# Kernel optimization log

Measured on AMD Instinct MI355X. Metric: run time of the kernel, lower is better.

## Reference

```python
import jax, jax.numpy as jnp
import numpy as np


def _he_scale(k, shape, fan_in):
    return jax.random.normal(k, shape, dtype=jnp.float32) * np.sqrt(2.0 / fan_in).astype(np.float32)


def setup_inputs() -> dict:
    key = jax.random.key(0)
    kx, kt, kp, kg, kf = jax.random.split(key, 5)
    B, H, W, C, D = 4, 64, 64, 256, 128
    x = jax.random.normal(kx, (B, H, W, C), dtype=jnp.float32)
    Wt = _he_scale(kt, (C, D), C)
    Wp = _he_scale(kp, (C, D), C)
    Wg = _he_scale(kg, (C, D), C)
    Wf = _he_scale(kf, (D, C), D)
    return {"x": x, "Wt": Wt, "Wp": Wp, "Wg": Wg, "Wf": Wf}


def _maxpool1d(z, pool_size=2, stride=1):
    # Keras MaxPool1D, padding='valid': output length = (N - pool_size)//stride + 1
    return jax.lax.reduce_window(
        z, -jnp.inf, jax.lax.max,
        window_dimensions=(1, pool_size, 1),
        window_strides=(1, stride, 1),
        padding='VALID')


def reference(x, Wt, Wp, Wg, Wf):
    B, H, W, C = x.shape
    D = Wt.shape[1]
    N = H * W
    # 1x1 conv projections == per-position matmuls
    theta = jnp.einsum('bhwc,cd->bhwd', x, Wt).reshape(B, N, D)   # [B,N,D]
    phi = jnp.einsum('bhwc,cd->bhwd', x, Wp).reshape(B, N, D)     # [B,N,D]
    g = jnp.einsum('bhwc,cd->bhwd', x, Wg).reshape(B, N, D)       # [B,N,D]
    # embedded mode: subsample phi and g (pool_size=2, strides=1) -> M = N-1
    phi = _maxpool1d(phi)                                          # [B,M,D]
    g = _maxpool1d(g)                                              # [B,M,D]
    # f = theta @ phi^T, softmax over keys (no scaling in embedded mode)
    f = jax.nn.softmax(jnp.einsum('bnd,bmd->bnm', theta, phi), axis=-1)  # [B,N,M]
    y = jnp.einsum('bnm,bmd->bnd', f, g).reshape(B, H, W, D)       # [B,H,W,D]
    # final 1x1 conv back to C channels + residual
    z = x + jnp.einsum('bhwd,dc->bhwc', y, Wf)
    return z
```

## Files before the change

### kernel.cpp

```cpp
#include <hip/hip_runtime.h>

#define B_  4
#define N_  4096
#define C_  256
#define D_  128
#define M_  4095
#define BN_ (B_ * N_)
#define KSPLIT 4
#define KEYS_PER_SPLIT (N_ / KSPLIT)
#define KTILES (KEYS_PER_SPLIT / 64)

typedef _Float16 half_t;
typedef __attribute__((ext_vector_type(8))) _Float16 half8;
typedef __attribute__((ext_vector_type(4))) _Float16 half4;
typedef __attribute__((ext_vector_type(4))) float f32x4;

#define MFMA16x16x32(A, B, C) __builtin_amdgcn_mfma_f32_16x16x32_f16(A, B, C, 0, 0, 0)
#define LOG2E 1.44269504088896f

__global__ __launch_bounds__(256) void prep_kernel(
    const float* __restrict__ Wt, const float* __restrict__ Wp,
    const float* __restrict__ Wg, const float* __restrict__ Wf,
    half_t* __restrict__ WT_hi, half_t* __restrict__ WT_lo,
    half_t* __restrict__ WfT)
{
    const int idx = blockIdx.x * 256 + threadIdx.x;
    const int wsel = blockIdx.y;
    if (wsel < 3) {
        const float* __restrict__ W = (wsel == 0) ? Wt : (wsel == 1) ? Wp : Wg;
        const int d = idx >> 8, c = idx & 255;
        const float v = W[(size_t)c * D_ + d];
        const half_t h = (half_t)v;
        WT_hi[(size_t)wsel * 32768 + idx] = h;
        WT_lo[(size_t)wsel * 32768 + idx] = (half_t)(v - (float)h);
    } else {
        const int c = idx >> 7, d = idx & 127;
        WfT[idx] = (half_t)Wf[(size_t)d * C_ + c];
    }
}

__global__ __launch_bounds__(256) void proj_kernel(
    const float* __restrict__ x, const half_t* __restrict__ WT_hi,
    const half_t* __restrict__ WT_lo, half_t* __restrict__ theta,
    half_t* __restrict__ pphi, half_t* __restrict__ pgT)
{
    const int tid = threadIdx.x;
    const int lane = tid & 63;
    const int w = tid >> 6;
    const int lm = lane & 15;
    const int lq = lane >> 4;
    const int r0 = blockIdx.x * 128;
    const int which = blockIdx.y;
    const half_t* __restrict__ Wh_g = WT_hi + (size_t)which * 32768;
    const half_t* __restrict__ Wl_g = WT_lo + (size_t)which * 32768;

    __shared__ __align__(16) unsigned char lds_raw[40960];
    half_t (*Xh)[40]  = (half_t (*)[40])(lds_raw);
    half_t (*Xl)[40]  = (half_t (*)[40])(lds_raw + 10240);
    half_t (*Whl)[40] = (half_t (*)[40])(lds_raw + 20480);
    half_t (*Wll)[40] = (half_t (*)[40])(lds_raw + 30720);

    f32x4 acc[2][8];
#pragma unroll
    for (int rb = 0; rb < 2; ++rb)
#pragma unroll
        for (int nb = 0; nb < 8; ++nb)
#pragma unroll
            for (int r = 0; r < 4; ++r) acc[rb][nb][r] = 0.f;

    const int sr = tid >> 1;
    const int cL = (tid & 1) * 16;

    for (int kc = 0; kc < 8; ++kc) {
        __syncthreads();
        {
            const float* xs = x + (size_t)(r0 + sr) * C_ + kc * 32 + cL;
            float vv[16];
            float4 v0 = *(const float4*)&xs[0], v1 = *(const float4*)&xs[4];
            float4 v2 = *(const float4*)&xs[8], v3 = *(const float4*)&xs[12];
            vv[0]=v0.x; vv[1]=v0.y; vv[2]=v0.z; vv[3]=v0.w;
            vv[4]=v1.x; vv[5]=v1.y; vv[6]=v1.z; vv[7]=v1.w;
            vv[8]=v2.x; vv[9]=v2.y; vv[10]=v2.z; vv[11]=v2.w;
            vv[12]=v3.x; vv[13]=v3.y; vv[14]=v3.z; vv[15]=v3.w;
            half8 hi[2], lo[2];
#pragma unroll
            for (int j = 0; j < 16; ++j) {
                half_t h = (half_t)vv[j];
                hi[j >> 3][j & 7] = h;
                lo[j >> 3][j & 7] = (half_t)(vv[j] - (float)h);
            }
            *(half8*)&Xh[sr][cL] = hi[0]; *(half8*)&Xh[sr][cL + 8] = hi[1];
            *(half8*)&Xl[sr][cL] = lo[0]; *(half8*)&Xl[sr][cL + 8] = lo[1];
            const half_t* wh = Wh_g + (size_t)sr * 256 + kc * 32 + cL;
            const half_t* wl = Wl_g + (size_t)sr * 256 + kc * 32 + cL;
            *(half8*)&Whl[sr][cL] = *(const half8*)&wh[0];
            *(half8*)&Whl[sr][cL + 8] = *(const half8*)&wh[8];
            *(half8*)&Wll[sr][cL] = *(const half8*)&wl[0];
            *(half8*)&Wll[sr][cL + 8] = *(const half8*)&wl[8];
        }
        __syncthreads();

        half8 ah[2], al[2];
#pragma unroll
        for (int rb = 0; rb < 2; ++rb) {
            ah[rb] = *(const half8*)&Xh[w * 32 + rb * 16 + lm][lq * 8];
            al[rb] = *(const half8*)&Xl[w * 32 + rb * 16 + lm][lq * 8];
        }
#pragma unroll
        for (int nb = 0; nb < 8; ++nb) {
            half8 bh = *(const half8*)&Whl[nb * 16 + lm][lq * 8];
            half8 bl = *(const half8*)&Wll[nb * 16 + lm][lq * 8];
#pragma unroll
            for (int rb = 0; rb < 2; ++rb) {
                acc[rb][nb] = MFMA16x16x32(ah[rb], bh, acc[rb][nb]);
                acc[rb][nb] = MFMA16x16x32(al[rb], bh, acc[rb][nb]);
                acc[rb][nb] = MFMA16x16x32(ah[rb], bl, acc[rb][nb]);
            }
        }
    }

    if (which == 0) {
#pragma unroll
        for (int rb = 0; rb < 2; ++rb)
#pragma unroll
            for (int nb = 0; nb < 8; ++nb)
#pragma unroll
                for (int r = 0; r < 4; ++r)
                    theta[(size_t)(r0 + w * 32 + rb * 16 + lq * 4 + r) * D_ +
                          nb * 16 + lm] = (half_t)(acc[rb][nb][r] * LOG2E);
        return;
    }

    __syncthreads();
    half_t (*LsT)[136] = (half_t (*)[136])(lds_raw);
#pragma unroll
    for (int rb = 0; rb < 2; ++rb)
#pragma unroll
        for (int nb = 0; nb < 8; ++nb) {
            const int d = nb * 16 + lm;
            const int m = w * 32 + rb * 16 + lq * 4;
            half4 pk;
#pragma unroll
            for (int r = 0; r < 4; ++r) pk[r] = (half_t)acc[rb][nb][r];
            *(half4*)&LsT[d][m] = pk;
        }
    if (tid < 128) {
        int rh = r0 + 128;
        if ((rh & (N_ - 1)) == 0) rh = r0 + 127;
        const float* xr = x + (size_t)rh * C_;
        const half_t* wh = Wh_g + (size_t)tid * 256;
        const half_t* wl = Wl_g + (size_t)tid * 256;
        float s = 0.f;
#pragma unroll
        for (int c8 = 0; c8 < 32; ++c8) {
            half8 h = *(const half8*)&wh[c8 * 8];
            half8 l = *(const half8*)&wl[c8 * 8];
            float4 xa = *(const float4*)&xr[c8 * 8];
            float4 xb = *(const float4*)&xr[c8 * 8 + 4];
            s += xa.x * ((float)h[0] + (float)l[0]) + xa.y * ((float)h[1] + (float)l[1])
               + xa.z * ((float)h[2] + (float)l[2]) + xa.w * ((float)h[3] + (float)l[3])
               + xb.x * ((float)h[4] + (float)l[4]) + xb.y * ((float)h[5] + (float)l[5])
               + xb.z * ((float)h[6] + (float)l[6]) + xb.w * ((float)h[7] + (float)l[7]);
        }
        LsT[tid][128] = (half_t)s;
    }
    __syncthreads();

    if (which == 1) {
        const int m = tid >> 1, dh = (tid & 1) * 64;
        half8 o[8];
#pragma unroll
        for (int j = 0; j < 64; ++j) {
            float v0 = (float)LsT[dh + j][m];
            float v1 = (float)LsT[dh + j][m + 1];
            o[j >> 3][j & 7] = (half_t)fmaxf(v0, v1);
        }
        half8* dst = (half8*)&pphi[(size_t)(r0 + m) * D_ + dh];
#pragma unroll
        for (int j = 0; j < 8; ++j) dst[j] = o[j];
    } else {
        const int d = tid >> 1, mh = (tid & 1) * 64;
        const int b = r0 / N_, m0 = r0 & (N_ - 1);
        half8 in[8];
#pragma unroll
        for (int j = 0; j < 8; ++j) in[j] = *(const half8*)&LsT[d][mh + j * 8];
        const half_t ext = LsT[d][mh + 64];
        half8 o[8];
#pragma unroll
        for (int j = 0; j < 64; ++j) {
            float v0 = (float)in[j >> 3][j & 7];
            float v1 = (j == 63) ? (float)ext : (float)in[(j + 1) >> 3][(j + 1) & 7];
            o[j >> 3][j & 7] = (half_t)fmaxf(v0, v1);
        }
        half8* dst = (half8*)&pgT[((size_t)b * D_ + d) * N_ + m0 + mh];
#pragma unroll
        for (int j = 0; j < 8; ++j) dst[j] = o[j];
    }
}

__global__ __launch_bounds__(256, 2) void attn_kernel(
    const half_t* __restrict__ theta, const half_t* __restrict__ pphi,
    const half_t* __restrict__ pgT, half_t* __restrict__ ypart,
    float* __restrict__ mstat, float* __restrict__ lstat)
{
    const int tid = threadIdx.x;
    const int lane = tid & 63;
    const int w = tid >> 6;
    const int lm = lane & 15;
    const int lq = lane >> 4;
    const int qt = blockIdx.x, ksb = blockIdx.y, b = blockIdx.z;
    const int q0 = qt * 128;

    __shared__ half_t Ks[64][136];
    __shared__ half_t Gts[128][72];
    __shared__ half_t Ps[128][72];

    half8 qh[2][4];
#pragma unroll
    for (int nb = 0; nb < 2; ++nb) {
        const half_t* tr_ = theta + ((size_t)b * N_ + q0 + w * 32 + nb * 16 + lm) * D_;
#pragma unroll
        for (int k4 = 0; k4 < 4; ++k4)
            qh[nb][k4] = *(const half8*)(tr_ + k4 * 32 + lq * 8);
    }

    float m_i[2] = {-1e30f, -1e30f};
    float l_i[2] = {0.f, 0.f};
    f32x4 yacc[2][8];
#pragma unroll
    for (int mb = 0; mb < 2; ++mb)
#pragma unroll
        for (int dn = 0; dn < 8; ++dn)
#pragma unroll
            for (int r = 0; r < 4; ++r) yacc[mb][dn][r] = 0.f;

    for (int kt = 0; kt < KTILES; ++kt) {
        const int k0 = ksb * KEYS_PER_SPLIT + kt * 64;
        __syncthreads();
        {
            const int key = tid >> 2, ch = (tid & 3);
            const float4* src = (const float4*)(pphi +
                ((size_t)b * N_ + k0 + key) * D_ + ch * 32);
            float4 a0 = src[0], a1 = src[1], a2 = src[2], a3 = src[3];
            float4* dst = (float4*)&Ks[key][ch * 32];
            dst[0] = a0; dst[1] = a1; dst[2] = a2; dst[3] = a3;
            const int d = tid >> 1, kh = (tid & 1);
            const float4* gs = (const float4*)(pgT +
                ((size_t)b * D_ + d) * N_ + k0 + kh * 32);
            float4 g0 = gs[0], g1 = gs[1], g2 = gs[2], g3 = gs[3];
            float4* gd = (float4*)&Gts[d][kh * 32];
            gd[0] = g0; gd[1] = g1; gd[2] = g2; gd[3] = g3;
        }
        __syncthreads();

        f32x4 sc[4][2];
#pragma unroll
        for (int kb = 0; kb < 4; ++kb)
#pragma unroll
            for (int nb = 0; nb < 2; ++nb)
#pragma unroll
                for (int r = 0; r < 4; ++r) sc[kb][nb][r] = 0.f;
#pragma unroll
        for (int kb = 0; kb < 4; ++kb) {
#pragma unroll
            for (int k4 = 0; k4 < 4; ++k4) {
                half8 kf = *(const half8*)&Ks[kb * 16 + lm][k4 * 32 + lq * 8];
#pragma unroll
                for (int nb = 0; nb < 2; ++nb)
                    sc[kb][nb] = MFMA16x16x32(kf, qh[nb][k4], sc[kb][nb]);
            }
        }
        if (k0 + 64 > M_) {
#pragma unroll
            for (int kb = 0; kb < 4; ++kb)
#pragma unroll
                for (int r = 0; r < 4; ++r)
                    if (k0 + kb * 16 + lq * 4 + r >= M_) {
                        sc[kb][0][r] = -1e30f; sc[kb][1][r] = -1e30f;
                    }
        }
        float alpha[2];
#pragma unroll
        for (int nb = 0; nb < 2; ++nb) {
            float mt = -1e30f;
#pragma unroll
            for (int kb = 0; kb < 4; ++kb)
#pragma unroll
                for (int r = 0; r < 4; ++r) mt = fmaxf(mt, sc[kb][nb][r]);
            mt = fmaxf(mt, __shfl_xor(mt, 16, 64));
            mt = fmaxf(mt, __shfl_xor(mt, 32, 64));
            const float mnew = fmaxf(m_i[nb], mt);
            alpha[nb] = exp2f(m_i[nb] - mnew);
            m_i[nb] = mnew;
            float rs = 0.f;
#pragma unroll
            for (int kb = 0; kb < 4; ++kb)
#pragma unroll
                for (int r = 0; r < 4; ++r) {
                    float p = exp2f(sc[kb][nb][r] - mnew);
                    sc[kb][nb][r] = p;
                    rs += p;
                }
            rs += __shfl_xor(rs, 16, 64);
            rs += __shfl_xor(rs, 32, 64);
            l_i[nb] = l_i[nb] * alpha[nb] + rs;
#pragma unroll
            for (int kb = 0; kb < 4; ++kb) {
                half4 pk;
#pragma unroll
                for (int r = 0; r < 4; ++r) pk[r] = (half_t)sc[kb][nb][r];
                *(half4*)&Ps[w * 32 + nb * 16 + lm][kb * 16 + lq * 4] = pk;
            }
        }
        float alpha_t[2][4];
#pragma unroll
        for (int mb = 0; mb < 2; ++mb)
#pragma unroll
            for (int r = 0; r < 4; ++r)
                alpha_t[mb][r] = __shfl(alpha[mb], lq * 4 + r, 16);
#pragma unroll
        for (int mb = 0; mb < 2; ++mb)
#pragma unroll
            for (int dn = 0; dn < 8; ++dn)
#pragma unroll
                for (int r = 0; r < 4; ++r) yacc[mb][dn][r] *= alpha_t[mb][r];
        half8 pf[2][2];
#pragma unroll
        for (int mb = 0; mb < 2; ++mb)
#pragma unroll
            for (int k2 = 0; k2 < 2; ++k2)
                pf[mb][k2] = *(const half8*)&Ps[w * 32 + mb * 16 + lm][k2 * 32 + lq * 8];
#pragma unroll
        for (int dn = 0; dn < 8; ++dn) {
#pragma unroll
            for (int k2 = 0; k2 < 2; ++k2) {
                half8 gf = *(const half8*)&Gts[dn * 16 + lm][k2 * 32 + lq * 8];
                yacc[0][dn] = MFMA16x16x32(pf[0][k2], gf, yacc[0][dn]);
                yacc[1][dn] = MFMA16x16x32(pf[1][k2], gf, yacc[1][dn]);
            }
        }
    }

    half_t* yp = ypart + ((size_t)ksb * BN_ + (size_t)b * N_) * D_;
#pragma unroll
    for (int mb = 0; mb < 2; ++mb)
#pragma unroll
        for (int dn = 0; dn < 8; ++dn)
#pragma unroll
            for (int r = 0; r < 4; ++r)
                yp[(size_t)(q0 + w * 32 + mb * 16 + lq * 4 + r) * D_ + dn * 16 + lm] =
                    (half_t)yacc[mb][dn][r];
    if (lq == 0) {
#pragma unroll
        for (int nb = 0; nb < 2; ++nb) {
            const int row = q0 + w * 32 + nb * 16 + lm;
            mstat[(size_t)ksb * BN_ + (size_t)b * N_ + row] = m_i[nb];
            lstat[(size_t)ksb * BN_ + (size_t)b * N_ + row] = l_i[nb];
        }
    }
}

__global__ __launch_bounds__(256) void final_kernel(
    const half_t* __restrict__ ypart, const float* __restrict__ mstat,
    const float* __restrict__ lstat, const float* __restrict__ x,
    const half_t* __restrict__ WfT, float* __restrict__ out)
{
    const int tid = threadIdx.x;
    const int lane = tid & 63;
    const int w = tid >> 6;
    const int lm = lane & 15;
    const int lq = lane >> 4;
    const int r0 = blockIdx.x * 128;
    const int c0 = blockIdx.y * 128;

    __shared__ half_t Ys[128][72];
    __shared__ half_t Wfs[128][72];
    __shared__ float scl[4][128];

    if (tid < 128) {
        const int row = r0 + tid;
        float mv[4], lv[4], wv[4];
        float Mx = -1e30f;
#pragma unroll
        for (int s = 0; s < 4; ++s) {
            mv[s] = mstat[(size_t)s * BN_ + row];
            lv[s] = lstat[(size_t)s * BN_ + row];
            Mx = fmaxf(Mx, mv[s]);
        }
        float lsum = 0.f;
#pragma unroll
        for (int s = 0; s < 4; ++s) { wv[s] = exp2f(mv[s] - Mx); lsum += wv[s] * lv[s]; }
        const float inv = 1.f / lsum;
#pragma unroll
        for (int s = 0; s < 4; ++s) scl[s][tid] = wv[s] * inv;
    }
    __syncthreads();

    f32x4 acc[2][8];
#pragma unroll
    for (int rb = 0; rb < 2; ++rb)
#pragma unroll
        for (int nb = 0; nb < 8; ++nb)
#pragma unroll
            for (int r = 0; r < 4; ++r) acc[rb][nb][r] = 0.f;

    const int sr = tid >> 1;
    const int dd = (tid & 1) * 32;

    for (int kc = 0; kc < 2; ++kc) {
        {
            const float s0 = scl[0][sr], s1 = scl[1][sr],
                        s2 = scl[2][sr], s3 = scl[3][sr];
            const size_t yb = (size_t)(r0 + sr) * D_ + kc * 64 + dd;
            half8 o[4];
#pragma unroll
            for (int q = 0; q < 4; ++q) {
                half8 y0 = *(const half8*)&ypart[0 * (size_t)BN_ * D_ + yb + q * 8];
                half8 y1 = *(const half8*)&ypart[1 * (size_t)BN_ * D_ + yb + q * 8];
                half8 y2 = *(const half8*)&ypart[2 * (size_t)BN_ * D_ + yb + q * 8];
                half8 y3 = *(const half8*)&ypart[3 * (size_t)BN_ * D_ + yb + q * 8];
#pragma unroll
                for (int j = 0; j < 8; ++j)
                    o[q][j] = (half_t)(s0 * (float)y0[j] + s1 * (float)y1[j] +
                                       s2 * (float)y2[j] + s3 * (float)y3[j]);
            }
#pragma unroll
            for (int q = 0; q < 4; ++q) *(half8*)&Ys[sr][dd + q * 8] = o[q];
            const half_t* wf = WfT + (size_t)(c0 + sr) * D_ + kc * 64 + dd;
#pragma unroll
            for (int q = 0; q < 4; ++q)
                *(half8*)&Wfs[sr][dd + q * 8] = *(const half8*)&wf[q * 8];
        }
        __syncthreads();

        half8 af[2][2];
#pragma unroll
        for (int rb = 0; rb < 2; ++rb)
#pragma unroll
            for (int k2 = 0; k2 < 2; ++k2)
                af[rb][k2] = *(const half8*)&Ys[w * 32 + rb * 16 + lm][k2 * 32 + lq * 8];
#pragma unroll
        for (int nb = 0; nb < 8; ++nb) {
#pragma unroll
            for (int k2 = 0; k2 < 2; ++k2) {
                half8 bf = *(const half8*)&Wfs[nb * 16 + lm][k2 * 32 + lq * 8];
                acc[0][nb] = MFMA16x16x32(af[0][k2], bf, acc[0][nb]);
                acc[1][nb] = MFMA16x16x32(af[1][k2], bf, acc[1][nb]);
            }
        }
        __syncthreads();
    }
#pragma unroll
    for (int rb = 0; rb < 2; ++rb)
#pragma unroll
        for (int nb = 0; nb < 8; ++nb)
#pragma unroll
            for (int r = 0; r < 4; ++r) {
                const int row = r0 + w * 32 + rb * 16 + lq * 4 + r;
                const int col = c0 + nb * 16 + lm;
                out[(size_t)row * C_ + col] =
                    acc[rb][nb][r] + x[(size_t)row * C_ + col];
            }
}

extern "C" void kernel_launch(void* const* d_in, const int* in_sizes, int n_in,
                              void* d_out, int out_size, void* d_ws, size_t ws_size,
                              hipStream_t stream)
{
    const float* x  = (const float*)d_in[0];
    const float* Wt = (const float*)d_in[1];
    const float* Wp = (const float*)d_in[2];
    const float* Wg = (const float*)d_in[3];
    const float* Wf = (const float*)d_in[4];
    float* out = (float*)d_out;

    const size_t SEG = (size_t)BN_ * D_;
    float* ws     = (float*)d_ws;
    half_t* theta = (half_t*)ws;
    half_t* pphi  = (half_t*)(ws + SEG / 2);
    half_t* pgT   = (half_t*)(ws + SEG);
    half_t* ypart = (half_t*)(ws + SEG + SEG / 2);
    float* mstat  = ws + 3 * SEG + SEG / 2;
    float* lstat  = mstat + (size_t)KSPLIT * BN_;
    half_t* WT_hi = (half_t*)(lstat + (size_t)KSPLIT * BN_);
    half_t* WT_lo = WT_hi + 3 * 32768;
    half_t* WfT   = WT_lo + 3 * 32768;

    prep_kernel<<<dim3(128, 4), 256, 0, stream>>>(Wt, Wp, Wg, Wf, WT_hi, WT_lo, WfT);
    proj_kernel<<<dim3(BN_ / 128, 3), 256, 0, stream>>>(x, WT_hi, WT_lo,
                                                        theta, pphi, pgT);
    attn_kernel<<<dim3(N_ / 128, KSPLIT, B_), 256, 0, stream>>>(
        theta, pphi, pgT, ypart, mstat, lstat);
    final_kernel<<<dim3(BN_ / 128, 2), 256, 0, stream>>>(
        ypart, mstat, lstat, x, WfT, out);
}
```

Before: 187.7 us.

## Split attention keys six ways with uneven ranges and raise occupancy

Attention now splits the key range into six chunks instead of four. Chunk boundaries are computed from tile indices, so splits can be uneven (10 or 11 tiles each), which puts more blocks on the GPU. Launch bounds are raised to three blocks per SM, and the per-tile cross-lane row-sum reduction is deferred to a single reduction at the end. The combine kernel is generalized to KSPLIT partials, and the workspace layout grows to hold six partial outputs. The cost is more ypart memory traffic in the final kernel and possible register pressure at the higher occupancy target.

```diff
diff --git a/kernel.cpp b/kernel.cpp
--- a/kernel.cpp
+++ b/kernel.cpp
@@ -6,9 +6,7 @@
 #define D_  128
 #define M_  4095
 #define BN_ (B_ * N_)
-#define KSPLIT 4
-#define KEYS_PER_SPLIT (N_ / KSPLIT)
-#define KTILES (KEYS_PER_SPLIT / 64)
+#define KSPLIT 6
 
 typedef _Float16 half_t;
 typedef __attribute__((ext_vector_type(8))) _Float16 half8;
@@ -198,7 +196,7 @@
     }
 }
 
-__global__ __launch_bounds__(256, 2) void attn_kernel(
+__global__ __launch_bounds__(256, 3) void attn_kernel(
     const half_t* __restrict__ theta, const half_t* __restrict__ pphi,
     const half_t* __restrict__ pgT, half_t* __restrict__ ypart,
     float* __restrict__ mstat, float* __restrict__ lstat)
@@ -210,6 +208,8 @@
     const int lq = lane >> 4;
     const int qt = blockIdx.x, ksb = blockIdx.y, b = blockIdx.z;
     const int q0 = qt * 128;
+    const int kt0 = (64 * ksb) / KSPLIT;
+    const int kt1 = (64 * (ksb + 1)) / KSPLIT;
 
     __shared__ half_t Ks[64][136];
     __shared__ half_t Gts[128][72];
@@ -234,8 +234,8 @@
 #pragma unroll
             for (int r = 0; r < 4; ++r) yacc[mb][dn][r] = 0.f;
 
-    for (int kt = 0; kt < KTILES; ++kt) {
-        const int k0 = ksb * KEYS_PER_SPLIT + kt * 64;
+    for (int kt = kt0; kt < kt1; ++kt) {
+        const int k0 = kt * 64;
         __syncthreads();
         {
             const int key = tid >> 2, ch = (tid & 3);
@@ -301,8 +301,6 @@
                     sc[kb][nb][r] = p;
                     rs += p;
                 }
-            rs += __shfl_xor(rs, 16, 64);
-            rs += __shfl_xor(rs, 32, 64);
             l_i[nb] = l_i[nb] * alpha[nb] + rs;
 #pragma unroll
             for (int kb = 0; kb < 4; ++kb) {
@@ -341,6 +339,11 @@
         }
     }
 
+#pragma unroll
+    for (int nb = 0; nb < 2; ++nb) {
+        l_i[nb] += __shfl_xor(l_i[nb], 16, 64);
+        l_i[nb] += __shfl_xor(l_i[nb], 32, 64);
+    }
     half_t* yp = ypart + ((size_t)ksb * BN_ + (size_t)b * N_) * D_;
 #pragma unroll
     for (int mb = 0; mb < 2; ++mb)
@@ -375,24 +378,24 @@
 
     __shared__ half_t Ys[128][72];
     __shared__ half_t Wfs[128][72];
-    __shared__ float scl[4][128];
+    __shared__ float scl[KSPLIT][128];
 
     if (tid < 128) {
         const int row = r0 + tid;
-        float mv[4], lv[4], wv[4];
+        float mv[KSPLIT], lv[KSPLIT], wv[KSPLIT];
         float Mx = -1e30f;
 #pragma unroll
-        for (int s = 0; s < 4; ++s) {
+        for (int s = 0; s < KSPLIT; ++s) {
             mv[s] = mstat[(size_t)s * BN_ + row];
             lv[s] = lstat[(size_t)s * BN_ + row];
             Mx = fmaxf(Mx, mv[s]);
         }
         float lsum = 0.f;
 #pragma unroll
-        for (int s = 0; s < 4; ++s) { wv[s] = exp2f(mv[s] - Mx); lsum += wv[s] * lv[s]; }
+        for (int s = 0; s < KSPLIT; ++s) { wv[s] = exp2f(mv[s] - Mx); lsum += wv[s] * lv[s]; }
         const float inv = 1.f / lsum;
 #pragma unroll
-        for (int s = 0; s < 4; ++s) scl[s][tid] = wv[s] * inv;
+        for (int s = 0; s < KSPLIT; ++s) scl[s][tid] = wv[s] * inv;
     }
     __syncthreads();
 
@@ -409,20 +412,24 @@
 
     for (int kc = 0; kc < 2; ++kc) {
         {
-            const float s0 = scl[0][sr], s1 = scl[1][sr],
-                        s2 = scl[2][sr], s3 = scl[3][sr];
+            float ss[KSPLIT];
+#pragma unroll
+            for (int s = 0; s < KSPLIT; ++s) ss[s] = scl[s][sr];
             const size_t yb = (size_t)(r0 + sr) * D_ + kc * 64 + dd;
             half8 o[4];
 #pragma unroll
             for (int q = 0; q < 4; ++q) {
-                half8 y0 = *(const half8*)&ypart[0 * (size_t)BN_ * D_ + yb + q * 8];
-                half8 y1 = *(const half8*)&ypart[1 * (size_t)BN_ * D_ + yb + q * 8];
-                half8 y2 = *(const half8*)&ypart[2 * (size_t)BN_ * D_ + yb + q * 8];
-                half8 y3 = *(const half8*)&ypart[3 * (size_t)BN_ * D_ + yb + q * 8];
-#pragma unroll
-                for (int j = 0; j < 8; ++j)
-                    o[q][j] = (half_t)(s0 * (float)y0[j] + s1 * (float)y1[j] +
-                                       s2 * (float)y2[j] + s3 * (float)y3[j]);
+                float m[8];
+#pragma unroll
+                for (int j = 0; j < 8; ++j) m[j] = 0.f;
+#pragma unroll
+                for (int s = 0; s < KSPLIT; ++s) {
+                    half8 yv = *(const half8*)&ypart[(size_t)s * BN_ * D_ + yb + q * 8];
+#pragma unroll
+                    for (int j = 0; j < 8; ++j) m[j] += ss[s] * (float)yv[j];
+                }
+#pragma unroll
+                for (int j = 0; j < 8; ++j) o[q][j] = (half_t)m[j];
             }
 #pragma unroll
             for (int q = 0; q < 4; ++q) *(half8*)&Ys[sr][dd + q * 8] = o[q];
@@ -480,7 +487,7 @@
     half_t* pphi  = (half_t*)(ws + SEG / 2);
     half_t* pgT   = (half_t*)(ws + SEG);
     half_t* ypart = (half_t*)(ws + SEG + SEG / 2);
-    float* mstat  = ws + 3 * SEG + SEG / 2;
+    float* mstat  = ws + SEG + SEG / 2 + 3 * SEG;
     float* lstat  = mstat + (size_t)KSPLIT * BN_;
     half_t* WT_hi = (half_t*)(lstat + (size_t)KSPLIT * BN_);
     half_t* WT_lo = WT_hi + 3 * 32768;
```

New measurement: 209.1 us. 11.4% more time.
